# Kernel tuning notes

Measured on AMD Instinct MI355X. Metric: run time of the kernel, lower is better.

The kernel has to match this reference:

```python
import jax, jax.numpy as jnp
import numpy as np
import math

N_HEAD = 12

def alibi_slopes(h):
    x = (2 ** 8) ** (1.0 / h)
    return jnp.array([1.0 / x ** (i + 1) for i in range(h)], dtype=jnp.float32)

def setup_inputs() -> dict:
    key = jax.random.key(0)
    k0, k1, k2 = jax.random.split(key, 3)
    B, T, C = 4, 2048, 576
    x = jax.random.normal(k0, (B, T, C), dtype=jnp.float32)
    w_qkv = jax.random.normal(k1, (3 * C, C), dtype=jnp.float32) * 0.02
    w_proj = jax.random.normal(k2, (C, C), dtype=jnp.float32) * 0.02
    return {"x": x, "w_qkv": w_qkv, "w_proj": w_proj}

def reference(x, w_qkv, w_proj):
    B, T, C = x.shape
    H = N_HEAD
    D = C // H
    qkv = x @ w_qkv.T  # [B,T,3C]
    q, k, v = jnp.split(qkv, 3, axis=2)
    q = q.reshape(B, T, H, D).transpose(0, 2, 1, 3)  # [B,H,T,D]
    k = k.reshape(B, T, H, D).transpose(0, 2, 1, 3)
    v = v.reshape(B, T, H, D).transpose(0, 2, 1, 3)
    # value residual with v1=None: v = 0.5*v + 0.5*v = v (faithful no-op)
    scale = 1.0 / math.sqrt(D)
    att = jnp.einsum('bhid,bhjd->bhij', q, k) * scale  # [B,H,T,T]
    # ALiBi bias as written: (col - row).clamp(min=0) * slope (zero on causal part)
    col = jnp.arange(T, dtype=jnp.float32)[None, :]
    row = jnp.arange(T, dtype=jnp.float32)[:, None]
    bias = jnp.maximum(col - row, 0.0)[None, :, :] * alibi_slopes(H)[:, None, None]  # [H,T,T]
    att = att + bias[None]
    causal = (jnp.arange(T)[None, :] <= jnp.arange(T)[:, None])  # [T,T] lower-tri
    att = jnp.where(causal[None, None], att, -jnp.inf)
    att = jax.nn.softmax(att, axis=-1)
    y = jnp.einsum('bhij,bhjd->bhid', att, v)  # [B,H,T,D]
    y = y.transpose(0, 2, 1, 3).reshape(B, T, C)
    return y @ w_proj.T
```

## Files before the change

kernel.cpp:

```cpp
#include <hip/hip_runtime.h>
#include <math.h>

#define Bn 4
#define Tn 2048
#define Cn 576
#define Hn 12
#define Dn 48
#define Mn (Bn*Tn)

#define QSCALE (1.4426950408889634f * 0.14433756729740643f)

typedef short  short8  __attribute__((ext_vector_type(8)));
typedef float  floatx4 __attribute__((ext_vector_type(4)));
typedef unsigned short ushort_t;
typedef unsigned short ushort8_t __attribute__((ext_vector_type(8)));

static __device__ __forceinline__ unsigned short f2bf(float f) {
    union { float f; unsigned int u; } v; v.f = f;
    unsigned int r = v.u + 0x7FFFu + ((v.u >> 16) & 1u);
    return (unsigned short)(r >> 16);
}

static __device__ __forceinline__ unsigned int pack_trunc(float a, float b) {
    union { float f; unsigned int u; } ua, ub; ua.f = a; ub.f = b;
    return (ua.u >> 16) | (ub.u & 0xFFFF0000u);
}

static __device__ __forceinline__ void gload16(void* lds, const void* g) {
    __builtin_amdgcn_global_load_lds(
        (const __attribute__((address_space(1))) void*)g,
        (__attribute__((address_space(3))) void*)lds, 16, 0, 0);
}

template<int N> static __device__ __forceinline__ void vmgate() {
    if constexpr (N == 0)      asm volatile("s_waitcnt vmcnt(0)" ::: "memory");
    else if constexpr (N == 4) asm volatile("s_waitcnt vmcnt(4)" ::: "memory");
    else if constexpr (N == 8) asm volatile("s_waitcnt vmcnt(8)" ::: "memory");
}
static __device__ __forceinline__ void lgk0() {
    asm volatile("s_waitcnt lgkmcnt(0)" ::: "memory");
}
static __device__ __forceinline__ void barrier_fence() {
    asm volatile("" ::: "memory");
    __builtin_amdgcn_s_barrier();
    asm volatile("" ::: "memory");
}

template<int N> static __device__ __forceinline__ void wait_vm_lg() {
    if constexpr (N == 0)
        asm volatile("s_waitcnt vmcnt(0) lgkmcnt(0)" ::: "memory");
    else if constexpr (N == 3)
        asm volatile("s_waitcnt vmcnt(3) lgkmcnt(0)" ::: "memory");
    else if constexpr (N == 6)
        asm volatile("s_waitcnt vmcnt(6) lgkmcnt(0)" ::: "memory");
    else
        static_assert(N == -12345, "unsupported waitcnt immediate");
}

__global__ __launch_bounds__(256)
void cast3(const float* __restrict__ a, ushort_t* __restrict__ oa, int na4,
           const float* __restrict__ b, ushort_t* __restrict__ ob, int nb4,
           const float* __restrict__ c, ushort_t* __restrict__ oc, int nc4,
           ushort_t* __restrict__ zb)
{
    int i = blockIdx.x * 256 + threadIdx.x;
    if (blockIdx.x == 0 && threadIdx.x < 16) {
        float4 z = (float4){0.f, 0.f, 0.f, 0.f};
        ((float4*)zb)[threadIdx.x] = z;
    }
    const float* src; ushort_t* dst; int idx;
    if (i < na4)                  { src = a; dst = oa; idx = i; }
    else if (i < na4 + nb4)       { src = b; dst = ob; idx = i - na4; }
    else if (i < na4 + nb4 + nc4) { src = c; dst = oc; idx = i - na4 - nb4; }
    else return;
    float4 v = ((const float4*)src)[idx];
    ushort4 o;
    o.x = f2bf(v.x); o.y = f2bf(v.y); o.z = f2bf(v.z); o.w = f2bf(v.w);
    ((ushort4*)dst)[idx] = o;
}

__global__ __launch_bounds__(512)
void gemm_qkv(const ushort_t* __restrict__ A, const ushort_t* __restrict__ W,
              ushort_t* __restrict__ outb)
{
    __shared__ __align__(16) ushort_t Ls[8][8192];

    const int tid  = threadIdx.x;
    const int wave = tid >> 6;
    const int lane = tid & 63;
    const int m    = lane & 15;
    const int g    = lane >> 4;
    const int wr   = wave >> 2;
    const int wn   = wave & 3;

    const int bid  = blockIdx.x;
    const int xcd  = bid & 7;
    const int slot = bid >> 3;
    const int ng   = slot % 7;
    const int mg   = xcd + 8 * (slot / 7);
    const int m0   = mg * 256;
    const int n0g  = ng * 256;

    const int srow = lane >> 2;
    const int schk = (lane & 3) * 16;
    const char* aS0 = (const char*)A + (size_t)(m0  + (wave*2+0)*16 + srow) * (Cn*2) + schk;
    const char* aS1 = (const char*)A + (size_t)(m0  + (wave*2+1)*16 + srow) * (Cn*2) + schk;
    const char* bS0 = (const char*)W + (size_t)(n0g + (wave*2+0)*16 + srow) * (Cn*2) + schk;
    const char* bS1 = (const char*)W + (size_t)(n0g + (wave*2+1)*16 + srow) * (Cn*2) + schk;

    const int aoff = (wr * 128 + m) * 64 + g * 16;
    const int boff = (wn * 64  + m) * 64 + g * 16;

    floatx4 acc[8][4];
    #pragma unroll
    for (int i = 0; i < 8; ++i)
        #pragma unroll
        for (int j = 0; j < 4; ++j)
            acc[i][j] = (floatx4){0.f, 0.f, 0.f, 0.f};

    short8 af[8], bf01[2], bf23[2];

    auto stageA = [&](int s) {
        gload16(&Ls[s][(wave*2+0)*512], aS0); aS0 += 64;
        gload16(&Ls[s][(wave*2+1)*512], aS1); aS1 += 64;
    };
    auto stageB = [&](int s) {
        gload16(&Ls[s][(wave*2+0)*512], bS0); bS0 += 64;
        gload16(&Ls[s][(wave*2+1)*512], bS1); bS1 += 64;
    };
    auto loadA = [&](int s) {
        const char* base = (const char*)&Ls[s][0] + aoff;
        #pragma unroll
        for (int mf = 0; mf < 8; ++mf) af[mf] = *(const short8*)(base + mf * 1024);
    };
    auto loadB = [&](int s, int nf0, short8 (&bf)[2]) {
        const char* base = (const char*)&Ls[s][0] + boff;
        bf[0] = *(const short8*)(base + (nf0 + 0) * 1024);
        bf[1] = *(const short8*)(base + (nf0 + 1) * 1024);
    };
    auto mfma16 = [&](short8 (&bf)[2], int nf0) {
        __builtin_amdgcn_s_setprio(1);
        #pragma unroll
        for (int mf = 0; mf < 8; ++mf) {
            acc[mf][nf0]     = __builtin_amdgcn_mfma_f32_16x16x32_bf16(af[mf], bf[0], acc[mf][nf0],     0, 0, 0);
            acc[mf][nf0 + 1] = __builtin_amdgcn_mfma_f32_16x16x32_bf16(af[mf], bf[1], acc[mf][nf0 + 1], 0, 0, 0);
        }
        __builtin_amdgcn_s_setprio(0);
    };

    stageA(0); stageB(1); stageA(2); stageB(3); stageA(4); stageB(5);
    vmgate<8>();
    barrier_fence();

    #define QKV_TILE(s0, d0, d1, d2, d3, G1m, G3m) do {                         \
        constexpr int A0 = (s0) & 7,      B0 = ((s0)+1) & 7;                    \
        constexpr int A1 = ((s0)+2) & 7,  B1 = ((s0)+3) & 7;                    \
        constexpr int S0 = ((s0)+6) & 7,  S1 = ((s0)+7) & 7;                    \
        constexpr int S2 = ((s0)+8) & 7,  S3 = ((s0)+9) & 7;                    \
        loadA(A0); loadB(B0, 0, bf01);                                          \
        if (d0) stageA(S0);                                                     \
        barrier_fence(); lgk0();                                                \
        mfma16(bf01, 0);                                                        \
        barrier_fence();                                                        \
        loadB(B0, 2, bf23);                                                     \
        if (d1) stageB(S1);                                                     \
        barrier_fence(); lgk0();                                                \
        mfma16(bf23, 2);                                                        \
        vmgate<G1m>();                                                          \
        barrier_fence();                                                        \
        loadA(A1); loadB(B1, 0, bf01);                                          \
        if (d2) stageA(S2);                                                     \
        barrier_fence(); lgk0();                                                \
        mfma16(bf01, 0);                                                        \
        barrier_fence();                                                        \
        loadB(B1, 2, bf23);                                                     \
        if (d3) stageB(S3);                                                     \
        barrier_fence(); lgk0();                                                \
        mfma16(bf23, 2);                                                        \
        vmgate<G3m>();                                                          \
        barrier_fence();                                                        \
    } while (0)

    #pragma unroll 1
    for (int tt = 0; tt < 3; ++tt) {
        QKV_TILE(0, 1, 1, 1, 1, 8, 8);
        QKV_TILE(4, 1, 1, 1, 1, 8, 8);
    }
    QKV_TILE(0, 1, 1, 1, 1, 8, 8);
    QKV_TILE(4, 1, 1, 0, 0, 8, 4);
    QKV_TILE(0, 0, 0, 0, 0, 0, -1);
    #undef QKV_TILE

    const size_t per = (size_t)Bn * Hn * Tn * Dn;
    const int b  = m0 >> 11;
    const int t0 = m0 & 2047;
    ushort_t* Lc = (ushort_t*)&Ls[0][0];

    #pragma unroll
    for (int h2 = 0; h2 < 2; ++h2) {
        const int  nbase = n0g + h2 * 128;
        const bool vmode = (nbase >= 1152);
        if ((wn >> 1) == h2) {
            if (!vmode) {
                #pragma unroll
                for (int mf = 0; mf < 8; ++mf)
                    #pragma unroll
                    for (int nf = 0; nf < 4; ++nf) {
                        const int  nfb = n0g + wn * 64 + nf * 16;
                        const float sc = (nfb < 576) ? QSCALE : 1.0f;
                        const int col = (wn & 1) * 64 + nf * 16 + m;
                        const int rb  = wr * 128 + mf * 16 + g * 4;
                        #pragma unroll
                        for (int r = 0; r < 4; ++r)
                            Lc[(rb + r) * 136 + col] = f2bf(acc[mf][nf][r] * sc);
                    }
            } else {
                #pragma unroll
                for (int mf = 0; mf < 8; ++mf)
                    #pragma unroll
                    for (int nf = 0; nf < 4; ++nf) {
                        const int col = (wn & 1) * 64 + nf * 16 + m;
                        const int rb  = wr * 128 + mf * 16 + g * 4;
                        ushort4 pk;
                        pk.x = f2bf(acc[mf][nf][0]); pk.y = f2bf(acc[mf][nf][1]);
                        pk.z = f2bf(acc[mf][nf][2]); pk.w = f2bf(acc[mf][nf][3]);
                        *(ushort4*)&Lc[col * 264 + rb] = pk;
                    }
            }
        }
        __syncthreads();
        if (!vmode) {
            #pragma unroll
            for (int it = 0; it < 8; ++it) {
                const int c   = tid + it * 512;
                const int row = c >> 4;
                const int c8  = (c & 15) * 8;
                const int n   = nbase + c8;
                const int which = (n >= 576);
                const int nn  = n - which * 576;
                const int h   = nn / 48, d = nn - h * 48;
                ushort_t* dst = outb + (size_t)which * per
                    + ((size_t)(b * Hn + h) * Tn + t0 + row) * Dn + d;
                *(ushort8_t*)dst = *(const ushort8_t*)&Lc[row * 136 + c8];
            }
        } else {
            #pragma unroll
            for (int it = 0; it < 8; ++it) {
                const int c   = tid + it * 512;
                const int col = c >> 5;
                const int rc  = (c & 31) * 8;
                const int n   = nbase + col;
                if (n < 1728) {
                    const int dd = n - 1152;
                    const int h  = dd / 48, d = dd - h * 48;
                    ushort_t* dst = outb + 2 * per
                        + ((size_t)(b * Hn + h) * Dn + d) * Tn + t0 + rc;
                    *(ushort8_t*)dst = *(const ushort8_t*)&Lc[col * 264 + rc];
                }
            }
        }
        __syncthreads();
    }
}

template<int MTILE>
__global__ __launch_bounds__(256)
void gemm_proj(const ushort_t* __restrict__ A, const ushort_t* __restrict__ W,
               float* __restrict__ outf)
{
    constexpr int SA   = MTILE / 16;
    constexpr int NSEG = SA + 4;
    constexpr int PW   = NSEG / 4;
    constexpr int MF   = MTILE / 64;
    constexpr int NB   = 9;
    constexpr int NST  = Cn / 32;
    constexpr int AH   = 2;
    constexpr int NBUF = 3;
    __shared__ __align__(16) ushort_t Ls[NBUF][NSEG][512];

    const int tid  = threadIdx.x;
    const int wave = tid >> 6;
    const int lane = tid & 63;
    const int m    = lane & 15;
    const int g    = lane >> 4;
    const int bid  = blockIdx.x;
    const int xcd  = bid & 7;
    const int slot = bid >> 3;
    const int n0   = (slot % NB) * 64;
    const int m0   = (xcd + 8 * (slot / NB)) * MTILE;

    floatx4 acc[MF][4];
    #pragma unroll
    for (int i = 0; i < MF; ++i)
        #pragma unroll
        for (int j = 0; j < 4; ++j)
            acc[i][j] = (floatx4){0.f, 0.f, 0.f, 0.f};

    const char* gp[PW];
    int         si[PW];
    #pragma unroll
    for (int i = 0; i < PW; ++i) {
        int s = wave + i * 4;
        si[i] = s;
        gp[i] = (s < SA)
            ? (const char*)(A + (size_t)(m0 + s * 16 + m) * Cn + g * 8)
            : (const char*)(W + (size_t)(n0 + (s - SA) * 16 + m) * Cn + g * 8);
    }

    #pragma unroll
    for (int s = 0; s < AH; ++s)
        #pragma unroll
        for (int i = 0; i < PW; ++i) { gload16(&Ls[s][si[i]][0], gp[i]); gp[i] += 64; }
    wait_vm_lg<(AH - 1) * PW>();
    __builtin_amdgcn_s_barrier();

    int buf  = 0;
    int sbuf = AH;
    for (int j = 0; j < NST; ++j) {
        if (j + AH < NST) {
            #pragma unroll
            for (int i = 0; i < PW; ++i) {
                gload16(&Ls[sbuf][si[i]][0], gp[i]);
                gp[i] += 64;
            }
        }
        short8 bf4[4];
        #pragma unroll
        for (int jj = 0; jj < 4; ++jj)
            bf4[jj] = *(const short8*)&Ls[buf][SA + jj][lane * 8];
        #pragma unroll
        for (int i = 0; i < MF; ++i) {
            short8 afr = *(const short8*)&Ls[buf][wave * MF + i][lane * 8];
            #pragma unroll
            for (int jj = 0; jj < 4; ++jj)
                acc[i][jj] = __builtin_amdgcn_mfma_f32_16x16x32_bf16(afr, bf4[jj], acc[i][jj], 0, 0, 0);
        }
        if (j < NST - AH) wait_vm_lg<(AH - 1) * PW>();
        else              wait_vm_lg<0>();
        __builtin_amdgcn_s_barrier();
        buf  = (buf  == NBUF - 1) ? 0 : buf  + 1;
        sbuf = (sbuf == NBUF - 1) ? 0 : sbuf + 1;
    }

    #pragma unroll
    for (int i = 0; i < MF; ++i) {
        #pragma unroll
        for (int r = 0; r < 4; ++r) {
            int mrow = m0 + wave * (MTILE / 4) + i * 16 + g * 4 + r;
            #pragma unroll
            for (int j = 0; j < 4; ++j)
                outf[(size_t)mrow * Cn + n0 + j * 16 + m] = acc[i][j][r];
        }
    }
}

__global__ __launch_bounds__(512, 6)
void attn_mfma(const ushort_t* __restrict__ Q, const ushort_t* __restrict__ K,
               const ushort_t* __restrict__ V, ushort_t* __restrict__ Y,
               const ushort_t* __restrict__ zb)
{
    __shared__ __align__(16) ushort_t QPs[16][512];
    __shared__ __align__(16) ushort_t Ks[2][8][512];
    __shared__ __align__(16) ushort_t Vs[2][6][512];

    const int id   = blockIdx.x;
    const int kk   = id / 48;
    const int bh   = id - kk * 48;
    const int QT   = (kk & 1) ? (kk >> 1) : (15 - (kk >> 1));
    const int tid  = threadIdx.x;
    const int wave = tid >> 6;
    const int lane = tid & 63;
    const int m    = lane & 15;
    const int g    = lane >> 4;
    const int q0   = QT * 128;
    const int nkt  = 2 * QT + 2;

    const ushort_t* Qp = Q + (size_t)bh * Tn * Dn;
    const ushort_t* Kp = K + (size_t)bh * Tn * Dn;
    const ushort_t* Vp = V + (size_t)bh * Dn * Tn;

    {
        const char* qrp = (const char*)(Qp + (size_t)(q0 + wave * 16 + m) * Dn);
        gload16(&QPs[wave * 2 + 0][0], qrp + g * 16);
        gload16(&QPs[wave * 2 + 1][0], (g < 2) ? (qrp + 64 + g * 16) : (const char*)zb);
    }

    const bool  kpad = ((wave & 1) == 1) && (g >= 2);
    const char* kptr = kpad ? (const char*)zb
        : (const char*)(Kp + (size_t)((wave >> 1) * 16 + m) * Dn) + (wave & 1) * 64 + g * 16;
    const int   kadv = kpad ? 0 : 64 * Dn * 2;
    const char* vptr = (const char*)(Vp + (size_t)((wave >> 1) * 16 + m) * Tn)
                       + (wave & 1) * 64 + g * 16;
    const int   vadv = 64 * 2;

    gload16(&Ks[0][wave][0], kptr); kptr += kadv;
    if (wave < 6) { gload16(&Vs[0][wave][0], vptr); vptr += vadv; }
    __syncthreads();

    short8 bq[2];
    bq[0] = *(const short8*)&QPs[wave * 2 + 0][lane * 8];
    bq[1] = *(const short8*)&QPs[wave * 2 + 1][lane * 8];

    floatx4 acc[3];
    #pragma unroll
    for (int t = 0; t < 3; ++t) acc[t] = (floatx4){0.f, 0.f, 0.f, 0.f};
    float l_tot = 0.f;
    const int qrow  = q0 + wave * 16 + m;
    const int qwmin = q0 + wave * 16;
    const int qwmax = qwmin + 15;

    for (int jt = 0; jt < nkt; ++jt) {
        const int cur = jt & 1;
        const int j0  = jt * 64;
        if (jt + 1 < nkt) {
            gload16(&Ks[cur ^ 1][wave][0], kptr); kptr += kadv;
            if (wave < 6) { gload16(&Vs[cur ^ 1][wave][0], vptr); vptr += vadv; }
        }

        if (j0 <= qwmax) {
            floatx4 s[4];
            #pragma unroll
            for (int t = 0; t < 4; ++t) {
                s[t] = (floatx4){0.f, 0.f, 0.f, 0.f};
                #pragma unroll
                for (int kc = 0; kc < 2; ++kc) {
                    short8 ak = *(const short8*)&Ks[cur][t * 2 + kc][lane * 8];
                    s[t] = __builtin_amdgcn_mfma_f32_16x16x32_bf16(ak, bq[kc], s[t], 0, 0, 0);
                }
            }

            float p[4][4];
            float lsum = 0.f;
            if (j0 + 63 > qwmin) {
                #pragma unroll
                for (int t = 0; t < 4; ++t)
                    #pragma unroll
                    for (int r = 0; r < 4; ++r) {
                        int j = j0 + t * 16 + g * 4 + r;
                        float v = (j <= qrow) ? s[t][r] : -1e30f;
                        float e = __builtin_amdgcn_exp2f(v);
                        p[t][r] = e; lsum += e;
                    }
            } else {
                #pragma unroll
                for (int t = 0; t < 4; ++t)
                    #pragma unroll
                    for (int r = 0; r < 4; ++r) {
                        float e = __builtin_amdgcn_exp2f(s[t][r]);
                        p[t][r] = e; lsum += e;
                    }
            }
            lsum += __shfl_xor(lsum, 16);
            lsum += __shfl_xor(lsum, 32);
            l_tot += lsum;

            #pragma unroll
            for (int t = 0; t < 4; ++t) {
                uint2 w2;
                w2.x = pack_trunc(p[t][0], p[t][1]);
                w2.y = pack_trunc(p[t][2], p[t][3]);
                *(uint2*)&QPs[wave * 2 + (t >> 1)]
                             [(2 * (t & 1) + (g >> 1)) * 128 + m * 8 + (g & 1) * 4] = w2;
            }
            asm volatile("s_waitcnt lgkmcnt(0)" ::: "memory");

            #pragma unroll
            for (int kc = 0; kc < 2; ++kc) {
                short8 bp = *(const short8*)&QPs[wave * 2 + kc][lane * 8];
                #pragma unroll
                for (int t = 0; t < 3; ++t) {
                    short8 av = *(const short8*)&Vs[cur][t * 2 + kc][lane * 8];
                    acc[t] = __builtin_amdgcn_mfma_f32_16x16x32_bf16(av, bp, acc[t], 0, 0, 0);
                }
            }
        }

        __syncthreads();
    }

    const float inv = 1.0f / l_tot;
    const int b = bh / Hn;
    const int h = bh - b * Hn;
    ushort_t* yp = Y + ((size_t)(b * Tn + qrow)) * Cn + h * Dn;
    #pragma unroll
    for (int t = 0; t < 3; ++t) {
        ushort4 o;
        o.x = f2bf(acc[t][0] * inv);
        o.y = f2bf(acc[t][1] * inv);
        o.z = f2bf(acc[t][2] * inv);
        o.w = f2bf(acc[t][3] * inv);
        *(ushort4*)&yp[t * 16 + g * 4] = o;
    }
}

extern "C" void kernel_launch(void* const* d_in, const int* in_sizes, int n_in,
                              void* d_out, int out_size, void* d_ws, size_t ws_size,
                              hipStream_t stream)
{
    const float* x      = (const float*)d_in[0];
    const float* w_qkv  = (const float*)d_in[1];
    const float* w_proj = (const float*)d_in[2];
    float* out = (float*)d_out;

    const size_t per = (size_t)Bn * Hn * Tn * Dn;

    ushort_t* xb  = (ushort_t*)d_ws;
    ushort_t* wqb = xb  + (size_t)Mn * Cn;
    ushort_t* wpb = wqb + (size_t)3 * Cn * Cn;
    ushort_t* qkv = wpb + (size_t)Cn * Cn;
    ushort_t* yb  = qkv + 3 * per;
    ushort_t* zb  = yb  + (size_t)Mn * Cn;

    const int na4 = Mn * Cn / 4, nb4 = 3 * Cn * Cn / 4, nc4 = Cn * Cn / 4;
    cast3<<<dim3((na4 + nb4 + nc4 + 255) / 256), dim3(256), 0, stream>>>(
        x, xb, na4, w_qkv, wqb, nb4, w_proj, wpb, nc4, zb);

    gemm_qkv<<<dim3(224), dim3(512), 0, stream>>>(xb, wqb, qkv);

    attn_mfma<<<dim3((Tn / 128) * Bn * Hn), dim3(512), 0, stream>>>(
        qkv, qkv + per, qkv + 2 * per, yb, zb);

    gemm_proj<128><<<dim3((Mn / 128) * 9), dim3(256), 0, stream>>>(yb, wpb, out);
}
```

Before: 163.7 us.

## Process two 16-row query tiles per wave in attention, halving block threads

The attention kernel now launches 256 threads (4 waves) per block instead of 512, and each wave handles 32 query rows as two 16-row sub-tiles. Each K fragment read from LDS now feeds two MFMAs, and each V fragment feeds two PV MFMAs, cutting LDS reads per unit of work. Global loads of K and V are spread over fewer waves. The cost is higher register pressure from doubled accumulators and score tiles, with the occupancy hint dropped from launch_bounds. Causal skipping is coarser, now per 32 rows.

```diff
diff --git a/kernel.cpp b/kernel.cpp
--- a/kernel.cpp
+++ b/kernel.cpp
@@ -354,7 +354,7 @@
     }
 }
 
-__global__ __launch_bounds__(512, 6)
+__global__ __launch_bounds__(256)
 void attn_mfma(const ushort_t* __restrict__ Q, const ushort_t* __restrict__ K,
                const ushort_t* __restrict__ V, ushort_t* __restrict__ Y,
                const ushort_t* __restrict__ zb)
@@ -368,7 +368,7 @@
     const int bh   = id - kk * 48;
     const int QT   = (kk & 1) ? (kk >> 1) : (15 - (kk >> 1));
     const int tid  = threadIdx.x;
-    const int wave = tid >> 6;
+    const int w    = tid >> 6;
     const int lane = tid & 63;
     const int m    = lane & 15;
     const int g    = lane >> 4;
@@ -380,97 +380,126 @@
     const ushort_t* Vp = V + (size_t)bh * Dn * Tn;
 
     {
-        const char* qrp = (const char*)(Qp + (size_t)(q0 + wave * 16 + m) * Dn);
-        gload16(&QPs[wave * 2 + 0][0], qrp + g * 16);
-        gload16(&QPs[wave * 2 + 1][0], (g < 2) ? (qrp + 64 + g * 16) : (const char*)zb);
-    }
-
-    const bool  kpad = ((wave & 1) == 1) && (g >= 2);
-    const char* kptr = kpad ? (const char*)zb
-        : (const char*)(Kp + (size_t)((wave >> 1) * 16 + m) * Dn) + (wave & 1) * 64 + g * 16;
-    const int   kadv = kpad ? 0 : 64 * Dn * 2;
-    const char* vptr = (const char*)(Vp + (size_t)((wave >> 1) * 16 + m) * Tn)
-                       + (wave & 1) * 64 + g * 16;
-    const int   vadv = 64 * 2;
-
-    gload16(&Ks[0][wave][0], kptr); kptr += kadv;
-    if (wave < 6) { gload16(&Vs[0][wave][0], vptr); vptr += vadv; }
+        #pragma unroll
+        for (int h2 = 0; h2 < 2; ++h2) {
+            const char* qrp = (const char*)(Qp + (size_t)(q0 + (w * 2 + h2) * 16 + m) * Dn);
+            gload16(&QPs[w * 4 + h2 * 2 + 0][0], qrp + g * 16);
+            gload16(&QPs[w * 4 + h2 * 2 + 1][0], (g < 2) ? (qrp + 64 + g * 16) : (const char*)zb);
+        }
+    }
+
+    const bool  kpad  = ((w & 1) == 1) && (g >= 2);
+    const char* kptrA = kpad ? (const char*)zb
+        : (const char*)(Kp + (size_t)((w >> 1) * 16 + m) * Dn) + (w & 1) * 64 + g * 16;
+    const char* kptrB = kpad ? (const char*)zb
+        : (const char*)(Kp + (size_t)(((w >> 1) + 2) * 16 + m) * Dn) + (w & 1) * 64 + g * 16;
+    const int   kadv  = kpad ? 0 : 64 * Dn * 2;
+
+    const char* vptr0 = (const char*)(Vp + (size_t)((w >> 1) * 16 + m) * Tn)
+                        + (w & 1) * 64 + g * 16;
+    const char* vptr1 = (const char*)(Vp + (size_t)(((w >> 1) + 2) * 16 + m) * Tn)
+                        + (w & 1) * 64 + g * 16;
+    const int   vadv  = 64 * 2;
+
+    gload16(&Ks[0][w][0],     kptrA); kptrA += kadv;
+    gload16(&Ks[0][w + 4][0], kptrB); kptrB += kadv;
+    gload16(&Vs[0][w][0], vptr0); vptr0 += vadv;
+    if (w < 2) { gload16(&Vs[0][w + 4][0], vptr1); vptr1 += vadv; }
     __syncthreads();
 
-    short8 bq[2];
-    bq[0] = *(const short8*)&QPs[wave * 2 + 0][lane * 8];
-    bq[1] = *(const short8*)&QPs[wave * 2 + 1][lane * 8];
-
-    floatx4 acc[3];
-    #pragma unroll
-    for (int t = 0; t < 3; ++t) acc[t] = (floatx4){0.f, 0.f, 0.f, 0.f};
-    float l_tot = 0.f;
-    const int qrow  = q0 + wave * 16 + m;
-    const int qwmin = q0 + wave * 16;
-    const int qwmax = qwmin + 15;
+    short8 bq[2][2];
+    #pragma unroll
+    for (int h2 = 0; h2 < 2; ++h2) {
+        bq[h2][0] = *(const short8*)&QPs[w * 4 + h2 * 2 + 0][lane * 8];
+        bq[h2][1] = *(const short8*)&QPs[w * 4 + h2 * 2 + 1][lane * 8];
+    }
+
+    floatx4 acc0[3], acc1[3];
+    #pragma unroll
+    for (int t = 0; t < 3; ++t) {
+        acc0[t] = (floatx4){0.f, 0.f, 0.f, 0.f};
+        acc1[t] = (floatx4){0.f, 0.f, 0.f, 0.f};
+    }
+    float lt0 = 0.f, lt1 = 0.f;
+    const int qrow0 = q0 + w * 32 + m;
+    const int qrow1 = qrow0 + 16;
+    const int qw0   = q0 + w * 32;
+    const int qwmax = qw0 + 31;
 
     for (int jt = 0; jt < nkt; ++jt) {
         const int cur = jt & 1;
         const int j0  = jt * 64;
         if (jt + 1 < nkt) {
-            gload16(&Ks[cur ^ 1][wave][0], kptr); kptr += kadv;
-            if (wave < 6) { gload16(&Vs[cur ^ 1][wave][0], vptr); vptr += vadv; }
+            gload16(&Ks[cur ^ 1][w][0],     kptrA); kptrA += kadv;
+            gload16(&Ks[cur ^ 1][w + 4][0], kptrB); kptrB += kadv;
+            gload16(&Vs[cur ^ 1][w][0], vptr0); vptr0 += vadv;
+            if (w < 2) { gload16(&Vs[cur ^ 1][w + 4][0], vptr1); vptr1 += vadv; }
         }
 
         if (j0 <= qwmax) {
-            floatx4 s[4];
+            floatx4 s0[4], s1[4];
             #pragma unroll
             for (int t = 0; t < 4; ++t) {
-                s[t] = (floatx4){0.f, 0.f, 0.f, 0.f};
+                s0[t] = (floatx4){0.f, 0.f, 0.f, 0.f};
+                s1[t] = (floatx4){0.f, 0.f, 0.f, 0.f};
                 #pragma unroll
                 for (int kc = 0; kc < 2; ++kc) {
                     short8 ak = *(const short8*)&Ks[cur][t * 2 + kc][lane * 8];
-                    s[t] = __builtin_amdgcn_mfma_f32_16x16x32_bf16(ak, bq[kc], s[t], 0, 0, 0);
+                    s0[t] = __builtin_amdgcn_mfma_f32_16x16x32_bf16(ak, bq[0][kc], s0[t], 0, 0, 0);
+                    s1[t] = __builtin_amdgcn_mfma_f32_16x16x32_bf16(ak, bq[1][kc], s1[t], 0, 0, 0);
                 }
             }
 
-            float p[4][4];
-            float lsum = 0.f;
-            if (j0 + 63 > qwmin) {
+            float l0 = 0.f, l1 = 0.f;
+            if (j0 + 63 > qw0) {
                 #pragma unroll
                 for (int t = 0; t < 4; ++t)
                     #pragma unroll
                     for (int r = 0; r < 4; ++r) {
-                        int j = j0 + t * 16 + g * 4 + r;
-                        float v = (j <= qrow) ? s[t][r] : -1e30f;
-                        float e = __builtin_amdgcn_exp2f(v);
-                        p[t][r] = e; lsum += e;
+                        const int j = j0 + t * 16 + g * 4 + r;
+                        float v0 = (j <= qrow0) ? s0[t][r] : -1e30f;
+                        float v1 = (j <= qrow1) ? s1[t][r] : -1e30f;
+                        float e0 = __builtin_amdgcn_exp2f(v0);
+                        float e1 = __builtin_amdgcn_exp2f(v1);
+                        s0[t][r] = e0; l0 += e0;
+                        s1[t][r] = e1; l1 += e1;
                     }
             } else {
                 #pragma unroll
                 for (int t = 0; t < 4; ++t)
                     #pragma unroll
                     for (int r = 0; r < 4; ++r) {
-                        float e = __builtin_amdgcn_exp2f(s[t][r]);
-                        p[t][r] = e; lsum += e;
+                        float e0 = __builtin_amdgcn_exp2f(s0[t][r]);
+                        float e1 = __builtin_amdgcn_exp2f(s1[t][r]);
+                        s0[t][r] = e0; l0 += e0;
+                        s1[t][r] = e1; l1 += e1;
                     }
             }
-            lsum += __shfl_xor(lsum, 16);
-            lsum += __shfl_xor(lsum, 32);
-            l_tot += lsum;
+            l0 += __shfl_xor(l0, 16); l0 += __shfl_xor(l0, 32); lt0 += l0;
+            l1 += __shfl_xor(l1, 16); l1 += __shfl_xor(l1, 32); lt1 += l1;
 
             #pragma unroll
             for (int t = 0; t < 4; ++t) {
-                uint2 w2;
-                w2.x = pack_trunc(p[t][0], p[t][1]);
-                w2.y = pack_trunc(p[t][2], p[t][3]);
-                *(uint2*)&QPs[wave * 2 + (t >> 1)]
-                             [(2 * (t & 1) + (g >> 1)) * 128 + m * 8 + (g & 1) * 4] = w2;
+                const int off = (2 * (t & 1) + (g >> 1)) * 128 + m * 8 + (g & 1) * 4;
+                uint2 w2a, w2b;
+                w2a.x = pack_trunc(s0[t][0], s0[t][1]);
+                w2a.y = pack_trunc(s0[t][2], s0[t][3]);
+                w2b.x = pack_trunc(s1[t][0], s1[t][1]);
+                w2b.y = pack_trunc(s1[t][2], s1[t][3]);
+                *(uint2*)&QPs[w * 4 + (t >> 1)][off]     = w2a;
+                *(uint2*)&QPs[w * 4 + 2 + (t >> 1)][off] = w2b;
             }
             asm volatile("s_waitcnt lgkmcnt(0)" ::: "memory");
 
             #pragma unroll
             for (int kc = 0; kc < 2; ++kc) {
-                short8 bp = *(const short8*)&QPs[wave * 2 + kc][lane * 8];
+                short8 bp0 = *(const short8*)&QPs[w * 4 + kc][lane * 8];
+                short8 bp1 = *(const short8*)&QPs[w * 4 + 2 + kc][lane * 8];
                 #pragma unroll
                 for (int t = 0; t < 3; ++t) {
                     short8 av = *(const short8*)&Vs[cur][t * 2 + kc][lane * 8];
-                    acc[t] = __builtin_amdgcn_mfma_f32_16x16x32_bf16(av, bp, acc[t], 0, 0, 0);
+                    acc0[t] = __builtin_amdgcn_mfma_f32_16x16x32_bf16(av, bp0, acc0[t], 0, 0, 0);
+                    acc1[t] = __builtin_amdgcn_mfma_f32_16x16x32_bf16(av, bp1, acc1[t], 0, 0, 0);
                 }
             }
         }
@@ -478,18 +507,33 @@
         __syncthreads();
     }
 
-    const float inv = 1.0f / l_tot;
     const int b = bh / Hn;
     const int h = bh - b * Hn;
-    ushort_t* yp = Y + ((size_t)(b * Tn + qrow)) * Cn + h * Dn;
-    #pragma unroll
-    for (int t = 0; t < 3; ++t) {
-        ushort4 o;
-        o.x = f2bf(acc[t][0] * inv);
-        o.y = f2bf(acc[t][1] * inv);
-        o.z = f2bf(acc[t][2] * inv);
-        o.w = f2bf(acc[t][3] * inv);
-        *(ushort4*)&yp[t * 16 + g * 4] = o;
+    {
+        const float inv = 1.0f / lt0;
+        ushort_t* yp = Y + ((size_t)(b * Tn + qrow0)) * Cn + h * Dn;
+        #pragma unroll
+        for (int t = 0; t < 3; ++t) {
+            ushort4 o;
+            o.x = f2bf(acc0[t][0] * inv);
+            o.y = f2bf(acc0[t][1] * inv);
+            o.z = f2bf(acc0[t][2] * inv);
+            o.w = f2bf(acc0[t][3] * inv);
+            *(ushort4*)&yp[t * 16 + g * 4] = o;
+        }
+    }
+    {
+        const float inv = 1.0f / lt1;
+        ushort_t* yp = Y + ((size_t)(b * Tn + qrow1)) * Cn + h * Dn;
+        #pragma unroll
+        for (int t = 0; t < 3; ++t) {
+            ushort4 o;
+            o.x = f2bf(acc1[t][0] * inv);
+            o.y = f2bf(acc1[t][1] * inv);
+            o.z = f2bf(acc1[t][2] * inv);
+            o.w = f2bf(acc1[t][3] * inv);
+            *(ushort4*)&yp[t * 16 + g * 4] = o;
+        }
     }
 }
 
@@ -517,7 +561,7 @@
 
     gemm_qkv<<<dim3(224), dim3(512), 0, stream>>>(xb, wqb, qkv);
 
-    attn_mfma<<<dim3((Tn / 128) * Bn * Hn), dim3(512), 0, stream>>>(
+    attn_mfma<<<dim3((Tn / 128) * Bn * Hn), dim3(256), 0, stream>>>(
         qkv, qkv + per, qkv + 2 * per, yb, zb);
 
     gemm_proj<128><<<dim3((Mn / 128) * 9), dim3(256), 0, stream>>>(yb, wpb, out);
```

Result: slower. 170.5 us (+4.1%).

## Load K/V fragments directly from global memory per wave, drop LDS staging

Applied to the files above, without the earlier changes.

The attention kernel stops staging K and V tiles in shared memory with double buffering and block-wide barriers. Each wave now reads its MFMA K and V operands straight from global memory and runs its own loop count, so waves whose causal range ends early stop early. This removes the per-tile __syncthreads and LDS traffic, and the occupancy hint on the launch bounds is dropped. In exchange, K/V reuse across the 8 waves now depends on cache, global read traffic goes up, and load latency is no longer hidden by prefetch. There is also a concern that the K padding for the second MFMA k-chunk, which used zeros before, may now read past the 48-wide head row.

```diff
diff --git a/kernel.cpp b/kernel.cpp
--- a/kernel.cpp
+++ b/kernel.cpp
@@ -354,128 +354,114 @@
     }
 }
 
-__global__ __launch_bounds__(512, 6)
+__global__ __launch_bounds__(512)
 void attn_mfma(const ushort_t* __restrict__ Q, const ushort_t* __restrict__ K,
                const ushort_t* __restrict__ V, ushort_t* __restrict__ Y,
                const ushort_t* __restrict__ zb)
 {
     __shared__ __align__(16) ushort_t QPs[16][512];
-    __shared__ __align__(16) ushort_t Ks[2][8][512];
-    __shared__ __align__(16) ushort_t Vs[2][6][512];
 
     const int id   = blockIdx.x;
     const int kk   = id / 48;
     const int bh   = id - kk * 48;
     const int QT   = (kk & 1) ? (kk >> 1) : (15 - (kk >> 1));
     const int tid  = threadIdx.x;
-    const int wave = tid >> 6;
+    const int w    = tid >> 6;
     const int lane = tid & 63;
     const int m    = lane & 15;
     const int g    = lane >> 4;
     const int q0   = QT * 128;
-    const int nkt  = 2 * QT + 2;
 
     const ushort_t* Qp = Q + (size_t)bh * Tn * Dn;
     const ushort_t* Kp = K + (size_t)bh * Tn * Dn;
     const ushort_t* Vp = V + (size_t)bh * Dn * Tn;
 
     {
-        const char* qrp = (const char*)(Qp + (size_t)(q0 + wave * 16 + m) * Dn);
-        gload16(&QPs[wave * 2 + 0][0], qrp + g * 16);
-        gload16(&QPs[wave * 2 + 1][0], (g < 2) ? (qrp + 64 + g * 16) : (const char*)zb);
-    }
-
-    const bool  kpad = ((wave & 1) == 1) && (g >= 2);
-    const char* kptr = kpad ? (const char*)zb
-        : (const char*)(Kp + (size_t)((wave >> 1) * 16 + m) * Dn) + (wave & 1) * 64 + g * 16;
-    const int   kadv = kpad ? 0 : 64 * Dn * 2;
-    const char* vptr = (const char*)(Vp + (size_t)((wave >> 1) * 16 + m) * Tn)
-                       + (wave & 1) * 64 + g * 16;
-    const int   vadv = 64 * 2;
-
-    gload16(&Ks[0][wave][0], kptr); kptr += kadv;
-    if (wave < 6) { gload16(&Vs[0][wave][0], vptr); vptr += vadv; }
-    __syncthreads();
+        const char* qrp = (const char*)(Qp + (size_t)(q0 + w * 16 + m) * Dn);
+        gload16(&QPs[w * 2 + 0][0], qrp + g * 16);
+        gload16(&QPs[w * 2 + 1][0], (g < 2) ? (qrp + 64 + g * 16) : (const char*)zb);
+    }
+    vmgate<0>();
 
     short8 bq[2];
-    bq[0] = *(const short8*)&QPs[wave * 2 + 0][lane * 8];
-    bq[1] = *(const short8*)&QPs[wave * 2 + 1][lane * 8];
+    bq[0] = *(const short8*)&QPs[w * 2 + 0][lane * 8];
+    bq[1] = *(const short8*)&QPs[w * 2 + 1][lane * 8];
 
     floatx4 acc[3];
     #pragma unroll
     for (int t = 0; t < 3; ++t) acc[t] = (floatx4){0.f, 0.f, 0.f, 0.f};
     float l_tot = 0.f;
-    const int qrow  = q0 + wave * 16 + m;
-    const int qwmin = q0 + wave * 16;
-    const int qwmax = qwmin + 15;
-
-    for (int jt = 0; jt < nkt; ++jt) {
-        const int cur = jt & 1;
-        const int j0  = jt * 64;
-        if (jt + 1 < nkt) {
-            gload16(&Ks[cur ^ 1][wave][0], kptr); kptr += kadv;
-            if (wave < 6) { gload16(&Vs[cur ^ 1][wave][0], vptr); vptr += vadv; }
-        }
-
-        if (j0 <= qwmax) {
-            floatx4 s[4];
-            #pragma unroll
-            for (int t = 0; t < 4; ++t) {
-                s[t] = (floatx4){0.f, 0.f, 0.f, 0.f};
+    const int qrow  = q0 + w * 16 + m;
+    const int qwmin = q0 + w * 16;
+    const int nw    = ((qwmin + 15) >> 6) + 1;
+
+    const ushort_t* kptr = Kp + (size_t)m * Dn + g * 8;
+    const ushort_t* vb0 = Vp + (size_t)(m)      * Tn + g * 8;
+    const ushort_t* vb1 = Vp + (size_t)(16 + m) * Tn + g * 8;
+    const ushort_t* vb2 = Vp + (size_t)(32 + m) * Tn + g * 8;
+
+    for (int jt = 0; jt < nw; ++jt) {
+        const int j0 = jt * 64;
+
+        floatx4 s[4];
+        #pragma unroll
+        for (int t = 0; t < 4; ++t) {
+            s[t] = (floatx4){0.f, 0.f, 0.f, 0.f};
+            #pragma unroll
+            for (int kc = 0; kc < 2; ++kc) {
+                short8 ak = *(const short8*)(kptr + t * 16 * Dn + kc * 32);
+                s[t] = __builtin_amdgcn_mfma_f32_16x16x32_bf16(ak, bq[kc], s[t], 0, 0, 0);
+            }
+        }
+
+        float p[4][4];
+        float lsum = 0.f;
+        if (j0 + 63 > qwmin) {
+            #pragma unroll
+            for (int t = 0; t < 4; ++t)
                 #pragma unroll
-                for (int kc = 0; kc < 2; ++kc) {
-                    short8 ak = *(const short8*)&Ks[cur][t * 2 + kc][lane * 8];
-                    s[t] = __builtin_amdgcn_mfma_f32_16x16x32_bf16(ak, bq[kc], s[t], 0, 0, 0);
+                for (int r = 0; r < 4; ++r) {
+                    int j = j0 + t * 16 + g * 4 + r;
+                    float v = (j <= qrow) ? s[t][r] : -1e30f;
+                    float e = __builtin_amdgcn_exp2f(v);
+                    p[t][r] = e; lsum += e;
                 }
-            }
-
-            float p[4][4];
-            float lsum = 0.f;
-            if (j0 + 63 > qwmin) {
+        } else {
+            #pragma unroll
+            for (int t = 0; t < 4; ++t)
                 #pragma unroll
-                for (int t = 0; t < 4; ++t)
-                    #pragma unroll
-                    for (int r = 0; r < 4; ++r) {
-                        int j = j0 + t * 16 + g * 4 + r;
-                        float v = (j <= qrow) ? s[t][r] : -1e30f;
-                        float e = __builtin_amdgcn_exp2f(v);
-                        p[t][r] = e; lsum += e;
-                    }
-            } else {
-                #pragma unroll
-                for (int t = 0; t < 4; ++t)
-                    #pragma unroll
-                    for (int r = 0; r < 4; ++r) {
-                        float e = __builtin_amdgcn_exp2f(s[t][r]);
-                        p[t][r] = e; lsum += e;
-                    }
-            }
-            lsum += __shfl_xor(lsum, 16);
-            lsum += __shfl_xor(lsum, 32);
-            l_tot += lsum;
-
-            #pragma unroll
-            for (int t = 0; t < 4; ++t) {
-                uint2 w2;
-                w2.x = pack_trunc(p[t][0], p[t][1]);
-                w2.y = pack_trunc(p[t][2], p[t][3]);
-                *(uint2*)&QPs[wave * 2 + (t >> 1)]
-                             [(2 * (t & 1) + (g >> 1)) * 128 + m * 8 + (g & 1) * 4] = w2;
-            }
-            asm volatile("s_waitcnt lgkmcnt(0)" ::: "memory");
-
-            #pragma unroll
-            for (int kc = 0; kc < 2; ++kc) {
-                short8 bp = *(const short8*)&QPs[wave * 2 + kc][lane * 8];
-                #pragma unroll
-                for (int t = 0; t < 3; ++t) {
-                    short8 av = *(const short8*)&Vs[cur][t * 2 + kc][lane * 8];
-                    acc[t] = __builtin_amdgcn_mfma_f32_16x16x32_bf16(av, bp, acc[t], 0, 0, 0);
+                for (int r = 0; r < 4; ++r) {
+                    float e = __builtin_amdgcn_exp2f(s[t][r]);
+                    p[t][r] = e; lsum += e;
                 }
-            }
-        }
-
-        __syncthreads();
+        }
+        lsum += __shfl_xor(lsum, 16);
+        lsum += __shfl_xor(lsum, 32);
+        l_tot += lsum;
+
+        #pragma unroll
+        for (int t = 0; t < 4; ++t) {
+            uint2 w2;
+            w2.x = pack_trunc(p[t][0], p[t][1]);
+            w2.y = pack_trunc(p[t][2], p[t][3]);
+            *(uint2*)&QPs[w * 2 + (t >> 1)]
+                         [(2 * (t & 1) + (g >> 1)) * 128 + m * 8 + (g & 1) * 4] = w2;
+        }
+        asm volatile("s_waitcnt lgkmcnt(0)" ::: "memory");
+
+        #pragma unroll
+        for (int kc = 0; kc < 2; ++kc) {
+            short8 bp = *(const short8*)&QPs[w * 2 + kc][lane * 8];
+            short8 av0 = *(const short8*)(vb0 + kc * 32);
+            short8 av1 = *(const short8*)(vb1 + kc * 32);
+            short8 av2 = *(const short8*)(vb2 + kc * 32);
+            acc[0] = __builtin_amdgcn_mfma_f32_16x16x32_bf16(av0, bp, acc[0], 0, 0, 0);
+            acc[1] = __builtin_amdgcn_mfma_f32_16x16x32_bf16(av1, bp, acc[1], 0, 0, 0);
+            acc[2] = __builtin_amdgcn_mfma_f32_16x16x32_bf16(av2, bp, acc[2], 0, 0, 0);
+        }
+
+        kptr += 64 * Dn;
+        vb0  += 64; vb1 += 64; vb2 += 64;
     }
 
     const float inv = 1.0f / l_tot;
```

Result: slower. 245.9 us (+50.2%).
